# Kernel tuning notes

Measured on AMD Instinct MI355X. Metric: run time of the kernel, lower is better.

The kernel has to match this reference:

```python
import jax, jax.numpy as jnp
import numpy as np

D, NH, DH, NL, NP, NLAYERS, DFF = 256, 8, 32, 3, 4, 6, 1024
SHAPES = ((64, 64), (32, 32), (16, 16))  # (H, W) per level, strides 8/16/32 of a 512px image


def layer_norm(x, g, b):
    m = jnp.mean(x, -1, keepdims=True)
    v = jnp.mean((x - m) ** 2, -1, keepdims=True)
    return (x - m) * jax.lax.rsqrt(v + 1e-5) * g + b


def _ref_points():
    pts = []
    for (h, w) in SHAPES:
        ry = (jnp.arange(h, dtype=jnp.float32) + 0.5) / h
        rx = (jnp.arange(w, dtype=jnp.float32) + 0.5) / w
        yy, xx = jnp.meshgrid(ry, rx, indexing='ij')
        pts.append(jnp.stack([xx.reshape(-1), yy.reshape(-1)], -1))
    return jnp.concatenate(pts, 0)  # [Q, 2] (x, y) normalized; valid_ratios == 1


def _sample_level(value_l, loc, h, w):
    # value_l: [B, NH, h*w, DH]; loc: [B, Q, NH, NP, 2] normalized in [0,1]
    # grid_sample(align_corners=False, padding zeros): pixel = loc*size - 0.5
    B, Q = loc.shape[0], loc.shape[1]
    x = loc[..., 0] * w - 0.5
    y = loc[..., 1] * h - 0.5
    x0f = jnp.floor(x); y0f = jnp.floor(y)
    lx = x - x0f; ly = y - y0f
    x0 = x0f.astype(jnp.int32); y0 = y0f.astype(jnp.int32)
    out = jnp.zeros((B, NH, Q, NP, DH), value_l.dtype)
    corners = ((0, 0, (1 - lx) * (1 - ly)), (1, 0, lx * (1 - ly)),
               (0, 1, (1 - lx) * ly), (1, 1, lx * ly))
    for dx, dy, wgt in corners:
        xi = x0 + dx; yi = y0 + dy
        valid = ((xi >= 0) & (xi < w) & (yi >= 0) & (yi < h)).astype(value_l.dtype)
        idx = jnp.clip(yi, 0, h - 1) * w + jnp.clip(xi, 0, w - 1)        # [B,Q,NH,NP]
        idx_f = jnp.transpose(idx, (0, 2, 1, 3)).reshape(B, NH, Q * NP)
        v = jnp.take_along_axis(value_l, idx_f[..., None], axis=2)       # [B,NH,Q*NP,DH]
        v = v.reshape(B, NH, Q, NP, DH)
        w_f = jnp.transpose(wgt * valid, (0, 2, 1, 3))                   # [B,NH,Q,NP]
        out = out + v * w_f[..., None]
    return out


def setup_inputs():
    key = jax.random.key(0)
    ks = iter(jax.random.split(key, 64))
    d = {}
    B = 4
    for i, (h, w) in enumerate(SHAPES):
        d[f'src{i}'] = jax.random.normal(next(ks), (B, D, h, w), jnp.float32)
        d[f'pos{i}'] = jax.random.normal(next(ks), (B, D, h, w), jnp.float32) * 0.1
    s = 0.02
    p = lambda shape: jax.random.normal(next(ks), shape, jnp.float32) * s
    d['level_embed'] = p((NL, D))
    d['W_off'] = p((NLAYERS, D, NH * NL * NP * 2)); d['b_off'] = p((NLAYERS, NH * NL * NP * 2))
    d['W_attn'] = p((NLAYERS, D, NH * NL * NP));   d['b_attn'] = p((NLAYERS, NH * NL * NP))
    d['W_val'] = p((NLAYERS, D, D)); d['b_val'] = p((NLAYERS, D))
    d['W_out'] = p((NLAYERS, D, D)); d['b_out'] = p((NLAYERS, D))
    d['ln1_g'] = jnp.ones((NLAYERS, D)); d['ln1_b'] = jnp.zeros((NLAYERS, D))
    d['W_ff1'] = p((NLAYERS, D, DFF)); d['b_ff1'] = p((NLAYERS, DFF))
    d['W_ff2'] = p((NLAYERS, DFF, D)); d['b_ff2'] = p((NLAYERS, D))
    d['ln2_g'] = jnp.ones((NLAYERS, D)); d['ln2_b'] = jnp.zeros((NLAYERS, D))
    return d


def reference(src0, src1, src2, pos0, pos1, pos2, level_embed,
              W_off, b_off, W_attn, b_attn, W_val, b_val, W_out, b_out,
              ln1_g, ln1_b, W_ff1, b_ff1, W_ff2, b_ff2, ln2_g, ln2_b):
    srcs = (src0, src1, src2)
    poss = (pos0, pos1, pos2)
    B = src0.shape[0]
    # flatten levels: [B, C, H, W] -> [B, H*W, C]; add per-level embedding to pos
    src = jnp.concatenate([s.reshape(B, D, -1).transpose(0, 2, 1) for s in srcs], 1)
    pos = jnp.concatenate([poss[l].reshape(B, D, -1).transpose(0, 2, 1) + level_embed[l]
                           for l in range(NL)], 1)
    Q = src.shape[1]
    ref = _ref_points()  # [Q, 2]
    x = src
    for i in range(NLAYERS):
        q = x + pos
        off = (q @ W_off[i] + b_off[i]).reshape(B, Q, NH, NL, NP, 2)
        aw = jax.nn.softmax((q @ W_attn[i] + b_attn[i]).reshape(B, Q, NH, NL * NP), -1)
        aw = aw.reshape(B, Q, NH, NL, NP)
        val = (x @ W_val[i] + b_val[i]).reshape(B, Q, NH, DH)
        attn_out = jnp.zeros((B, Q, NH, DH), x.dtype)
        start = 0
        for l, (h, w) in enumerate(SHAPES):
            hw = h * w
            v_l = jnp.transpose(val[:, start:start + hw], (0, 2, 1, 3))  # [B,NH,hw,DH]
            wh = jnp.array([w, h], jnp.float32)
            loc = ref[None, :, None, None, :] + off[:, :, :, l] / wh     # [B,Q,NH,NP,2]
            smp = _sample_level(v_l, loc, h, w)                          # [B,NH,Q,NP,DH]
            attn_out = attn_out + jnp.einsum('bhqpd,bqhp->bqhd', smp, aw[:, :, :, l])
            start += hw
        attn_out = attn_out.reshape(B, Q, D) @ W_out[i] + b_out[i]
        x = layer_norm(x + attn_out, ln1_g[i], ln1_b[i])
        ff = jax.nn.relu(x @ W_ff1[i] + b_ff1[i]) @ W_ff2[i] + b_ff2[i]
        x = layer_norm(x + ff, ln2_g[i], ln2_b[i])
    return x  # memory: [B, Q, D]
```

## Files before the change

### kernel.cpp

```cpp
#include <hip/hip_runtime.h>


#define DMODEL 256
#define NLAYERS 6
#define BATCH 4
#define QTOT 5376
#define MROWS (BATCH * QTOT)

typedef __bf16 bf16x8 __attribute__((ext_vector_type(8)));
typedef __bf16 bf16x4 __attribute__((ext_vector_type(4)));
typedef float floatx4 __attribute__((ext_vector_type(4)));

__global__ __launch_bounds__(256) void flatten_kernel(
    const float* __restrict__ s0, const float* __restrict__ p0,
    const float* __restrict__ s1, const float* __restrict__ p1,
    const float* __restrict__ s2, const float* __restrict__ p2,
    const float* __restrict__ lvl, float* __restrict__ x,
    float* __restrict__ pos, __bf16* __restrict__ xb,
    __bf16* __restrict__ qb) {
  __shared__ float ls[32][33];
  __shared__ float lp[32][33];
  int b = blockIdx.y;
  int tile = blockIdx.x;
  const float* sp; const float* pp; int l, hw, tp, td, qbase;
  if (tile < 1024)      { l = 0; hw = 4096; int t = tile;        td = t & 7; tp = t >> 3; qbase = 0; sp = s0; pp = p0; }
  else if (tile < 1280) { l = 1; hw = 1024; int t = tile - 1024; td = t & 7; tp = t >> 3; qbase = 4096; sp = s1; pp = p1; }
  else                  { l = 2; hw = 256;  int t = tile - 1280; td = t & 7; tp = t >> 3; qbase = 5120; sp = s2; pp = p2; }
  int tx = threadIdx.x & 31, ty = threadIdx.x >> 5;
  int d0 = td * 32, pbase = tp * 32;
#pragma unroll
  for (int r = 0; r < 4; ++r) {
    int dl = r * 8 + ty;
    size_t gi = ((size_t)(b * DMODEL + d0 + dl)) * hw + pbase + tx;
    ls[dl][tx] = sp[gi];
    lp[dl][tx] = pp[gi];
  }
  __syncthreads();
  int d = d0 + tx;
  float lv = lvl[l * DMODEL + d];
#pragma unroll
  for (int r = 0; r < 4; ++r) {
    int pl = r * 8 + ty;
    size_t bq = (size_t)b * QTOT + qbase + pbase + pl;
    float xv = ls[tx][pl];
    float pv = lp[tx][pl] + lv;
    x[bq * DMODEL + d] = xv;
    xb[bq * DMODEL + d] = (__bf16)xv;
    pos[bq * DMODEL + d] = pv;
    qb[bq * DMODEL + d] = (__bf16)(xv + pv);
  }
}

__global__ __launch_bounds__(256) void pack_wt_kernel(
    const float* __restrict__ W, __bf16* __restrict__ Wt, int K, int N) {
  int l = blockIdx.y;
  int idx = blockIdx.x * 256 + threadIdx.x;
  int n = idx / K, k = idx - n * K;
  Wt[(size_t)l * N * K + idx] = (__bf16)W[(size_t)l * K * N + (size_t)k * N + n];
}

__global__ __launch_bounds__(256) void pack_qv_kernel(
    const float* __restrict__ Woff, const float* __restrict__ Wattn,
    const float* __restrict__ Wval,
    const float* __restrict__ boff, const float* __restrict__ battn,
    const float* __restrict__ bval,
    __bf16* __restrict__ Wt, float* __restrict__ bc) {
  int l = blockIdx.y;
  int n = blockIdx.x;
  int k = threadIdx.x;
  float v = 0.f;
  if (n < 192)      v = Woff[((size_t)l * 256 + k) * 192 + n];
  else if (n < 288) v = Wattn[((size_t)l * 256 + k) * 96 + (n - 192)];
  else if (n >= 384) v = Wval[((size_t)l * 256 + k) * 256 + (n - 384)];
  Wt[((size_t)l * 640 + n) * 256 + k] = (__bf16)v;
  if (k == 0) {
    float b = 0.f;
    if (n < 192)      b = boff[l * 192 + n];
    else if (n < 288) b = battn[l * 96 + (n - 192)];
    else if (n >= 384) b = bval[l * 256 + (n - 384)];
    bc[l * 640 + n] = b;
  }
}

#define GEMM_CORE(A_, B_, K_)                                                  \
  for (int k0 = 0; k0 < (K_); k0 += 32) {                                      \
    __syncthreads();                                                           \
    _Pragma("unroll")                                                          \
    for (int cc = 0; cc < 2; ++cc) {                                           \
      int c = wid * 2 + cc;                                                    \
      __builtin_amdgcn_global_load_lds(                                        \
          (__attribute__((address_space(1))) void*)((A_) + (size_t)c * 16 * (K_) + k0), \
          (__attribute__((address_space(3))) void*)(As + c * 512), 16, 0, 0);  \
      __builtin_amdgcn_global_load_lds(                                        \
          (__attribute__((address_space(1))) void*)((B_) + (size_t)c * 16 * (K_) + k0), \
          (__attribute__((address_space(3))) void*)(Bs + c * 512), 16, 0, 0);  \
    }                                                                          \
    __syncthreads();                                                           \
    bf16x8 af[4], bfr[4];                                                      \
    _Pragma("unroll")                                                          \
    for (int i = 0; i < 4; ++i)                                                \
      af[i] = *(const bf16x8*)&As[(wr * 64 + i * 16 + (lane & 15)) * 32 + (lane >> 4) * 8]; \
    _Pragma("unroll")                                                          \
    for (int j = 0; j < 4; ++j)                                                \
      bfr[j] = *(const bf16x8*)&Bs[(wc * 64 + j * 16 + (lane & 15)) * 32 + (lane >> 4) * 8]; \
    _Pragma("unroll")                                                          \
    for (int i = 0; i < 4; ++i)                                                \
      _Pragma("unroll")                                                        \
      for (int j = 0; j < 4; ++j)                                              \
        acc[i][j] = __builtin_amdgcn_mfma_f32_16x16x32_bf16(af[i], bfr[j], acc[i][j], 0, 0, 0); \
  }

template<int RELU, int BF16OUT>
__global__ __launch_bounds__(256) void gemm_bf16_kernel(
    const __bf16* __restrict__ A, const __bf16* __restrict__ Wt,
    const float* __restrict__ bias, float* __restrict__ C,
    __bf16* __restrict__ Cb, int N, int K) {
  __shared__ __bf16 As[128 * 32];
  __shared__ __bf16 Bs[128 * 32];
  int t = threadIdx.x;
  int lane = t & 63, wid = t >> 6;
  int wr = wid >> 1, wc = wid & 1;
  int row0 = blockIdx.y * 128;
  int n0 = blockIdx.x * 128;
  floatx4 acc[4][4] = {};
  int srow = lane >> 2;
  int skoff = (lane & 3) * 8;
  const __bf16* Abase = A + (size_t)(row0 + srow) * K + skoff;
  const __bf16* Bbase = Wt + (size_t)(n0 + srow) * K + skoff;
  GEMM_CORE(Abase, Bbase, K)
  int orow = row0 + wr * 64 + (lane >> 4) * 4;
  int ocol = n0 + wc * 64 + (lane & 15);
#pragma unroll
  for (int i = 0; i < 4; ++i)
#pragma unroll
    for (int j = 0; j < 4; ++j) {
      int col = ocol + j * 16;
      float bv = bias[col];
#pragma unroll
      for (int r = 0; r < 4; ++r) {
        int row = orow + i * 16 + r;
        float v = acc[i][j][r] + bv;
        if (RELU) v = fmaxf(v, 0.f);
        if (BF16OUT) Cb[(size_t)row * N + col] = (__bf16)v;
        else         C[(size_t)row * N + col] = v;
      }
    }
}

__global__ __launch_bounds__(256) void gemm_qv_kernel(
    const __bf16* __restrict__ qb, const __bf16* __restrict__ xb,
    const __bf16* __restrict__ Wt, const float* __restrict__ bias,
    float* __restrict__ qproj, __bf16* __restrict__ valb) {
  __shared__ __bf16 As[128 * 32];
  __shared__ __bf16 Bs[128 * 32];
  int t = threadIdx.x;
  int lane = t & 63, wid = t >> 6;
  int wr = wid >> 1, wc = wid & 1;
  int bn = blockIdx.x;
  int row0 = blockIdx.y * 128;
  int n0 = bn * 128;
  const __bf16* A = (bn < 3) ? qb : xb;
  floatx4 acc[4][4] = {};
  int srow = lane >> 2;
  int skoff = (lane & 3) * 8;
  const __bf16* Abase = A + (size_t)(row0 + srow) * 256 + skoff;
  const __bf16* Bbase = Wt + (size_t)(n0 + srow) * 256 + skoff;
  GEMM_CORE(Abase, Bbase, 256)
  int orow = row0 + wr * 64 + (lane >> 4) * 4;
  int ocol = wc * 64 + (lane & 15);
#pragma unroll
  for (int i = 0; i < 4; ++i)
#pragma unroll
    for (int j = 0; j < 4; ++j) {
      int col = ocol + j * 16;
      float bv = bias[n0 + col];
#pragma unroll
      for (int r = 0; r < 4; ++r) {
        int row = orow + i * 16 + r;
        float v = acc[i][j][r] + bv;
        if (bn < 3) qproj[(size_t)row * 384 + n0 + col] = v;
        else        valb[(size_t)row * 256 + (n0 - 384) + col] = (__bf16)v;
      }
    }
}

__global__ __launch_bounds__(256) void deform_kernel(
    const __bf16* __restrict__ val, const float* __restrict__ qproj,
    __bf16* __restrict__ out) {
  int bq = blockIdx.x * 8 + (threadIdx.x >> 5);
  int b = bq / QTOT, q = bq % QTOT;
  int tq = threadIdx.x & 31;
  int hid = tq >> 2, dq = (tq & 3) * 8;

  int p, wsrc;
  if (q < 4096)      { p = q;        wsrc = 64; }
  else if (q < 5120) { p = q - 4096; wsrc = 32; }
  else               { p = q - 5120; wsrc = 16; }
  float inv = 1.0f / (float)wsrc;
  float refx = ((float)(p % wsrc) + 0.5f) * inv;
  float refy = ((float)(p / wsrc) + 0.5f) * inv;

  const float* base = qproj + (size_t)bq * 384;
  float aw[12], ob[24];
  *(float4*)&aw[0] = *(const float4*)(base + 192 + hid * 12);
  *(float4*)&aw[4] = *(const float4*)(base + 192 + hid * 12 + 4);
  *(float4*)&aw[8] = *(const float4*)(base + 192 + hid * 12 + 8);
#pragma unroll
  for (int i = 0; i < 6; ++i)
    *(float4*)&ob[i * 4] = *(const float4*)(base + hid * 24 + i * 4);

  float mx = -1e30f;
#pragma unroll
  for (int k = 0; k < 12; ++k) mx = fmaxf(mx, aw[k]);
  float s = 0.f;
#pragma unroll
  for (int k = 0; k < 12; ++k) { aw[k] = __expf(aw[k] - mx); s += aw[k]; }
  float invs = 1.0f / s;
#pragma unroll
  for (int k = 0; k < 12; ++k) aw[k] *= invs;

  const __bf16* vb = val + ((size_t)b * QTOT) * DMODEL + hid * 32 + dq;

  const int starts[3] = {0, 4096, 5120};
  const int wls[3] = {64, 32, 16};
  float acc[8] = {};
#pragma unroll
  for (int l = 0; l < 3; ++l) {
    int wl = wls[l], start = starts[l];
    float fwl = (float)wl;
#pragma unroll
    for (int pp = 0; pp < 4; ++pp) {
      float wcomb = aw[l * 4 + pp];
      float fx = refx * fwl + ob[(l * 4 + pp) * 2 + 0] - 0.5f;
      float fy = refy * fwl + ob[(l * 4 + pp) * 2 + 1] - 0.5f;
      float x0f = floorf(fx), y0f = floorf(fy);
      float lx = fx - x0f, ly = fy - y0f;
      int x0 = (int)x0f, y0 = (int)y0f;
#pragma unroll
      for (int c = 0; c < 4; ++c) {
        int dx = c & 1, dy = c >> 1;
        int xi = x0 + dx, yi = y0 + dy;
        if (xi >= 0 && xi < wl && yi >= 0 && yi < wl) {
          float wgt = (dx ? lx : 1.f - lx) * (dy ? ly : 1.f - ly) * wcomb;
          bf16x8 v = *(const bf16x8*)(vb + (size_t)(start + yi * wl + xi) * DMODEL);
#pragma unroll
          for (int e = 0; e < 8; ++e)
            acc[e] = fmaf(wgt, (float)v[e], acc[e]);
        }
      }
    }
  }
  bf16x8 o;
#pragma unroll
  for (int e = 0; e < 8; ++e) o[e] = (__bf16)acc[e];
  *(bf16x8*)(out + (size_t)bq * DMODEL + hid * 32 + dq) = o;
}

__global__ __launch_bounds__(256) void add_ln_kernel(
    const float* __restrict__ x, const float* __restrict__ res,
    const float* __restrict__ g, const float* __restrict__ bta,
    float* __restrict__ xout, __bf16* __restrict__ xb,
    const float* __restrict__ pos, __bf16* __restrict__ qb) {
  int row = blockIdx.x * 4 + (threadIdx.x >> 6);
  int lane = threadIdx.x & 63;
  float4 xv = ((const float4*)(x + (size_t)row * DMODEL))[lane];
  float4 rv = ((const float4*)(res + (size_t)row * DMODEL))[lane];
  xv.x += rv.x; xv.y += rv.y; xv.z += rv.z; xv.w += rv.w;
  float s = xv.x + xv.y + xv.z + xv.w;
  float sq = xv.x * xv.x + xv.y * xv.y + xv.z * xv.z + xv.w * xv.w;
#pragma unroll
  for (int o = 32; o >= 1; o >>= 1) {
    s += __shfl_xor(s, o);
    sq += __shfl_xor(sq, o);
  }
  float mean = s * (1.f / 256.f);
  float var = sq * (1.f / 256.f) - mean * mean;
  float rstd = rsqrtf(var + 1e-5f);
  int c = lane * 4;
  float4 gv = *(const float4*)(g + c);
  float4 bv = *(const float4*)(bta + c);
  float4 o4;
  o4.x = (xv.x - mean) * rstd * gv.x + bv.x;
  o4.y = (xv.y - mean) * rstd * gv.y + bv.y;
  o4.z = (xv.z - mean) * rstd * gv.z + bv.z;
  o4.w = (xv.w - mean) * rstd * gv.w + bv.w;
  ((float4*)(xout + (size_t)row * DMODEL))[lane] = o4;
  bf16x4 ob;
  ob[0] = (__bf16)o4.x; ob[1] = (__bf16)o4.y;
  ob[2] = (__bf16)o4.z; ob[3] = (__bf16)o4.w;
  *(bf16x4*)&xb[(size_t)row * DMODEL + c] = ob;
  if (pos) {
    float4 pv = ((const float4*)(pos + (size_t)row * DMODEL))[lane];
    bf16x4 qv;
    qv[0] = (__bf16)(o4.x + pv.x); qv[1] = (__bf16)(o4.y + pv.y);
    qv[2] = (__bf16)(o4.z + pv.z); qv[3] = (__bf16)(o4.w + pv.w);
    *(bf16x4*)&qb[(size_t)row * DMODEL + c] = qv;
  }
}

extern "C" void kernel_launch(void* const* d_in, const int* in_sizes, int n_in,
                              void* d_out, int out_size, void* d_ws, size_t ws_size,
                              hipStream_t stream) {
  const float* src0 = (const float*)d_in[0];
  const float* pos0 = (const float*)d_in[1];
  const float* src1 = (const float*)d_in[2];
  const float* pos1 = (const float*)d_in[3];
  const float* src2 = (const float*)d_in[4];
  const float* pos2 = (const float*)d_in[5];
  const float* lvl  = (const float*)d_in[6];
  const float* W_off  = (const float*)d_in[7];
  const float* b_off  = (const float*)d_in[8];
  const float* W_attn = (const float*)d_in[9];
  const float* b_attn = (const float*)d_in[10];
  const float* W_val  = (const float*)d_in[11];
  const float* b_val  = (const float*)d_in[12];
  const float* W_out  = (const float*)d_in[13];
  const float* b_out  = (const float*)d_in[14];
  const float* ln1g = (const float*)d_in[15];
  const float* ln1b = (const float*)d_in[16];
  const float* W_ff1 = (const float*)d_in[17];
  const float* b_ff1 = (const float*)d_in[18];
  const float* W_ff2 = (const float*)d_in[19];
  const float* b_ff2 = (const float*)d_in[20];
  const float* ln2g = (const float*)d_in[21];
  const float* ln2b = (const float*)d_in[22];

  const size_t M = (size_t)MROWS;
  char* w = (char*)d_ws;
  float*  x     = (float*)w;                 w += M * 256 * 4;
  float*  pos   = (float*)w;                 w += M * 256 * 4;
  __bf16* xb    = (__bf16*)w;                w += M * 256 * 2;
  __bf16* qb    = (__bf16*)w;                w += M * 256 * 2;
  float*  qproj = (float*)w;                 w += M * 384 * 4;
  __bf16* valb  = (__bf16*)w;                w += M * 256 * 2;
  __bf16* ffh   = (__bf16*)w;                w += M * 1024 * 2;
  __bf16* wqv_t = (__bf16*)w;                w += (size_t)NLAYERS * 640 * 256 * 2;
  __bf16* wout_t= (__bf16*)w;                w += (size_t)NLAYERS * 256 * 256 * 2;
  __bf16* wff1_t= (__bf16*)w;                w += (size_t)NLAYERS * 1024 * 256 * 2;
  __bf16* wff2_t= (__bf16*)w;                w += (size_t)NLAYERS * 256 * 1024 * 2;
  float*  bqv   = (float*)w;                 w += (size_t)NLAYERS * 640 * 4;
  __bf16* attn_bf = qb;
  float*  proj  = (float*)ffh;
  float*  ffres = qproj;

  pack_qv_kernel<<<dim3(640, NLAYERS), 256, 0, stream>>>(
      W_off, W_attn, W_val, b_off, b_attn, b_val, wqv_t, bqv);
  pack_wt_kernel<<<dim3(256, NLAYERS), 256, 0, stream>>>(W_out, wout_t, 256, 256);
  pack_wt_kernel<<<dim3(1024, NLAYERS), 256, 0, stream>>>(W_ff1, wff1_t, 256, 1024);
  pack_wt_kernel<<<dim3(1024, NLAYERS), 256, 0, stream>>>(W_ff2, wff2_t, 1024, 256);

  flatten_kernel<<<dim3(1344, BATCH), 256, 0, stream>>>(
      src0, pos0, src1, pos1, src2, pos2, lvl, x, pos, xb, qb);

  const int MT = MROWS / 128;
  for (int i = 0; i < NLAYERS; ++i) {
    gemm_qv_kernel<<<dim3(5, MT), 256, 0, stream>>>(
        qb, xb, wqv_t + (size_t)i * 640 * 256, bqv + i * 640, qproj, valb);
    deform_kernel<<<MROWS / 8, 256, 0, stream>>>(valb, qproj, attn_bf);
    gemm_bf16_kernel<0, 0><<<dim3(2, MT), 256, 0, stream>>>(
        attn_bf, wout_t + (size_t)i * 256 * 256, b_out + i * 256, proj, nullptr, 256, 256);
    add_ln_kernel<<<MROWS / 4, 256, 0, stream>>>(
        x, proj, ln1g + i * 256, ln1b + i * 256, x, xb, nullptr, nullptr);
    gemm_bf16_kernel<1, 1><<<dim3(8, MT), 256, 0, stream>>>(
        xb, wff1_t + (size_t)i * 1024 * 256, b_ff1 + i * 1024, nullptr, ffh, 1024, 256);
    gemm_bf16_kernel<0, 0><<<dim3(2, MT), 256, 0, stream>>>(
        ffh, wff2_t + (size_t)i * 256 * 1024, b_ff2 + i * 256, ffres, nullptr, 256, 1024);
    float* xdst = (i == NLAYERS - 1) ? (float*)d_out : x;
    add_ln_kernel<<<MROWS / 4, 256, 0, stream>>>(
        x, ffres, ln2g + i * 256, ln2b + i * 256, xdst, xb, pos, qb);
  }
}
```

Measured before the change: 1.017 ms.

## Fuse residual add and LayerNorm into full-row output GEMM epilogues

Replaces the out-projection and FF2 GEMMs plus their separate add+LayerNorm kernels with one kernel whose 64x256 tile covers a whole row. It adds bias and residual, reduces the row statistics across waves through LDS, and writes the fp32, bf16 and query outputs directly. This removes the fp32 intermediate round-trips and two launches per layer. The weight packing kernels are also rewritten as LDS-tiled transposes for coalesced access. The 64-row tiles give the output GEMMs a different occupancy and reuse balance, and xout may alias xin.

Measured after the change: 1.088 ms. 6.9% more time.

```diff
diff --git a/kernel.cpp b/kernel.cpp
--- a/kernel.cpp
+++ b/kernel.cpp
@@ -10,6 +10,11 @@
 typedef __bf16 bf16x8 __attribute__((ext_vector_type(8)));
 typedef __bf16 bf16x4 __attribute__((ext_vector_type(4)));
 typedef float floatx4 __attribute__((ext_vector_type(4)));
+
+#define GLOAD(gp, lp)                                                          \
+  __builtin_amdgcn_global_load_lds(                                            \
+      (__attribute__((address_space(1))) void*)(gp),                           \
+      (__attribute__((address_space(3))) void*)(lp), 16, 0, 0)
 
 __global__ __launch_bounds__(256) void flatten_kernel(
     const float* __restrict__ s0, const float* __restrict__ p0,
@@ -51,35 +56,54 @@
   }
 }
 
-__global__ __launch_bounds__(256) void pack_wt_kernel(
+__global__ __launch_bounds__(256) void pack_t_kernel(
     const float* __restrict__ W, __bf16* __restrict__ Wt, int K, int N) {
-  int l = blockIdx.y;
-  int idx = blockIdx.x * 256 + threadIdx.x;
-  int n = idx / K, k = idx - n * K;
-  Wt[(size_t)l * N * K + idx] = (__bf16)W[(size_t)l * K * N + (size_t)k * N + n];
-}
-
-__global__ __launch_bounds__(256) void pack_qv_kernel(
+  __shared__ float ls[32][33];
+  int l = blockIdx.z;
+  int n0 = blockIdx.x * 32, k0 = blockIdx.y * 32;
+  int tx = threadIdx.x & 31, ty = threadIdx.x >> 5;
+  const float* src = W + (size_t)l * K * N;
+#pragma unroll
+  for (int r = 0; r < 4; ++r)
+    ls[ty + r * 8][tx] = src[(size_t)(k0 + ty + r * 8) * N + n0 + tx];
+  __syncthreads();
+  __bf16* dst = Wt + (size_t)l * N * K;
+#pragma unroll
+  for (int r = 0; r < 4; ++r)
+    dst[(size_t)(n0 + ty + r * 8) * K + k0 + tx] = (__bf16)ls[tx][ty + r * 8];
+}
+
+__global__ __launch_bounds__(256) void pack_qv_t_kernel(
     const float* __restrict__ Woff, const float* __restrict__ Wattn,
-    const float* __restrict__ Wval,
+    const float* __restrict__ Wval, __bf16* __restrict__ Wt) {
+  __shared__ float ls[32][33];
+  int l = blockIdx.z;
+  int tc = blockIdx.x, k0 = blockIdx.y * 32;
+  int tx = threadIdx.x & 31, ty = threadIdx.x >> 5;
+  const float* src; int n0, sn;
+  if (tc < 6)       { src = Woff  + (size_t)l * 256 * 192; n0 = tc * 32;        sn = 192; }
+  else if (tc < 9)  { src = Wattn + (size_t)l * 256 * 96;  n0 = (tc - 6) * 32;  sn = 96;  }
+  else if (tc < 12) { src = nullptr; n0 = 0; sn = 0; }
+  else              { src = Wval  + (size_t)l * 256 * 256; n0 = (tc - 12) * 32; sn = 256; }
+#pragma unroll
+  for (int r = 0; r < 4; ++r)
+    ls[ty + r * 8][tx] = src ? src[(size_t)(k0 + ty + r * 8) * sn + n0 + tx] : 0.f;
+  __syncthreads();
+  __bf16* dst = Wt + (size_t)l * 640 * 256 + (size_t)tc * 32 * 256;
+#pragma unroll
+  for (int r = 0; r < 4; ++r)
+    dst[(size_t)(ty + r * 8) * 256 + k0 + tx] = (__bf16)ls[tx][ty + r * 8];
+}
+
+__global__ __launch_bounds__(640) void pack_bias_kernel(
     const float* __restrict__ boff, const float* __restrict__ battn,
-    const float* __restrict__ bval,
-    __bf16* __restrict__ Wt, float* __restrict__ bc) {
-  int l = blockIdx.y;
-  int n = blockIdx.x;
-  int k = threadIdx.x;
-  float v = 0.f;
-  if (n < 192)      v = Woff[((size_t)l * 256 + k) * 192 + n];
-  else if (n < 288) v = Wattn[((size_t)l * 256 + k) * 96 + (n - 192)];
-  else if (n >= 384) v = Wval[((size_t)l * 256 + k) * 256 + (n - 384)];
-  Wt[((size_t)l * 640 + n) * 256 + k] = (__bf16)v;
-  if (k == 0) {
-    float b = 0.f;
-    if (n < 192)      b = boff[l * 192 + n];
-    else if (n < 288) b = battn[l * 96 + (n - 192)];
-    else if (n >= 384) b = bval[l * 256 + (n - 384)];
-    bc[l * 640 + n] = b;
-  }
+    const float* __restrict__ bval, float* __restrict__ bc) {
+  int l = blockIdx.x, n = threadIdx.x;
+  float b = 0.f;
+  if (n < 192)       b = boff[l * 192 + n];
+  else if (n < 288)  b = battn[l * 96 + (n - 192)];
+  else if (n >= 384) b = bval[l * 256 + (n - 384)];
+  bc[l * 640 + n] = b;
 }
 
 #define GEMM_CORE(A_, B_, K_)                                                  \
@@ -88,12 +112,8 @@
     _Pragma("unroll")                                                          \
     for (int cc = 0; cc < 2; ++cc) {                                           \
       int c = wid * 2 + cc;                                                    \
-      __builtin_amdgcn_global_load_lds(                                        \
-          (__attribute__((address_space(1))) void*)((A_) + (size_t)c * 16 * (K_) + k0), \
-          (__attribute__((address_space(3))) void*)(As + c * 512), 16, 0, 0);  \
-      __builtin_amdgcn_global_load_lds(                                        \
-          (__attribute__((address_space(1))) void*)((B_) + (size_t)c * 16 * (K_) + k0), \
-          (__attribute__((address_space(3))) void*)(Bs + c * 512), 16, 0, 0);  \
+      GLOAD((A_) + (size_t)c * 16 * (K_) + k0, As + c * 512);                  \
+      GLOAD((B_) + (size_t)c * 16 * (K_) + k0, Bs + c * 512);                  \
     }                                                                          \
     __syncthreads();                                                           \
     bf16x8 af[4], bfr[4];                                                      \
@@ -184,6 +204,111 @@
     }
 }
 
+template<int QB, int KK>
+__global__ __launch_bounds__(256) void gemm_ln_kernel(
+    const __bf16* __restrict__ A, const __bf16* __restrict__ Wt,
+    const float* __restrict__ bias, const float* __restrict__ xin,
+    const float* __restrict__ g, const float* __restrict__ bta,
+    float* __restrict__ xout, __bf16* __restrict__ xb,
+    const float* __restrict__ pos, __bf16* __restrict__ qb) {
+  __shared__ __bf16 As[64 * 32];
+  __shared__ __bf16 Bs[256 * 32];
+  __shared__ float stats[64][2];
+  int t = threadIdx.x, lane = t & 63, wid = t >> 6;
+  int row0 = blockIdx.x * 64;
+  floatx4 acc[4][4] = {};
+  int srow = lane >> 2, skoff = (lane & 3) * 8;
+  const __bf16* Abase = A + (size_t)(row0 + srow) * KK + skoff;
+  const __bf16* Bbase = Wt + (size_t)srow * KK + skoff;
+
+  for (int k0 = 0; k0 < KK; k0 += 32) {
+    __syncthreads();
+#pragma unroll
+    for (int cc = 0; cc < 5; ++cc) {
+      int c = wid * 5 + cc;
+      if (c < 4) GLOAD(Abase + (size_t)c * 16 * KK + k0, As + c * 512);
+      else       GLOAD(Bbase + (size_t)(c - 4) * 16 * KK + k0, Bs + (c - 4) * 512);
+    }
+    __syncthreads();
+    bf16x8 af[4], bfr[4];
+#pragma unroll
+    for (int i = 0; i < 4; ++i)
+      af[i] = *(const bf16x8*)&As[(i * 16 + (lane & 15)) * 32 + (lane >> 4) * 8];
+#pragma unroll
+    for (int j = 0; j < 4; ++j)
+      bfr[j] = *(const bf16x8*)&Bs[(wid * 64 + j * 16 + (lane & 15)) * 32 + (lane >> 4) * 8];
+#pragma unroll
+    for (int i = 0; i < 4; ++i)
+#pragma unroll
+      for (int j = 0; j < 4; ++j)
+        acc[i][j] = __builtin_amdgcn_mfma_f32_16x16x32_bf16(af[i], bfr[j], acc[i][j], 0, 0, 0);
+  }
+
+  __syncthreads();
+  float* part = (float*)As;
+
+  int lr0 = (lane >> 4) * 4;
+  int colbase = wid * 64 + (lane & 15);
+  float psum[4][4] = {}, psq[4][4] = {};
+#pragma unroll
+  for (int i = 0; i < 4; ++i)
+#pragma unroll
+    for (int j = 0; j < 4; ++j) {
+      int col = colbase + j * 16;
+      float bv = bias[col];
+#pragma unroll
+      for (int r = 0; r < 4; ++r) {
+        int lr = lr0 + i * 16 + r;
+        float v = acc[i][j][r] + bv + xin[(size_t)(row0 + lr) * DMODEL + col];
+        acc[i][j][r] = v;
+        psum[i][r] += v;
+        psq[i][r] += v * v;
+      }
+    }
+#pragma unroll
+  for (int o = 1; o < 16; o <<= 1)
+#pragma unroll
+    for (int i = 0; i < 4; ++i)
+#pragma unroll
+      for (int r = 0; r < 4; ++r) {
+        psum[i][r] += __shfl_xor(psum[i][r], o);
+        psq[i][r]  += __shfl_xor(psq[i][r], o);
+      }
+  {
+    int m = lane & 15, i = m >> 2, r = m & 3;
+    int lr = lr0 + i * 16 + r;
+    part[lr * 8 + wid]     = psum[i][r];
+    part[lr * 8 + 4 + wid] = psq[i][r];
+  }
+  __syncthreads();
+  if (t < 64) {
+    float s = part[t * 8 + 0] + part[t * 8 + 1] + part[t * 8 + 2] + part[t * 8 + 3];
+    float q = part[t * 8 + 4] + part[t * 8 + 5] + part[t * 8 + 6] + part[t * 8 + 7];
+    float mean = s * (1.f / 256.f);
+    float var = q * (1.f / 256.f) - mean * mean;
+    stats[t][0] = mean;
+    stats[t][1] = rsqrtf(var + 1e-5f);
+  }
+  __syncthreads();
+#pragma unroll
+  for (int i = 0; i < 4; ++i)
+#pragma unroll
+    for (int j = 0; j < 4; ++j) {
+      int col = colbase + j * 16;
+      float gv = g[col], bv = bta[col];
+#pragma unroll
+      for (int r = 0; r < 4; ++r) {
+        int lr = lr0 + i * 16 + r;
+        float mean = stats[lr][0], rstd = stats[lr][1];
+        float o = (acc[i][j][r] - mean) * rstd * gv + bv;
+        size_t idx = (size_t)(row0 + lr) * DMODEL + col;
+        xout[idx] = o;
+        xb[idx] = (__bf16)o;
+        if (QB) qb[idx] = (__bf16)(o + pos[idx]);
+      }
+    }
+}
+
 __global__ __launch_bounds__(256) void deform_kernel(
     const __bf16* __restrict__ val, const float* __restrict__ qproj,
     __bf16* __restrict__ out) {
@@ -254,48 +379,6 @@
 #pragma unroll
   for (int e = 0; e < 8; ++e) o[e] = (__bf16)acc[e];
   *(bf16x8*)(out + (size_t)bq * DMODEL + hid * 32 + dq) = o;
-}
-
-__global__ __launch_bounds__(256) void add_ln_kernel(
-    const float* __restrict__ x, const float* __restrict__ res,
-    const float* __restrict__ g, const float* __restrict__ bta,
-    float* __restrict__ xout, __bf16* __restrict__ xb,
-    const float* __restrict__ pos, __bf16* __restrict__ qb) {
-  int row = blockIdx.x * 4 + (threadIdx.x >> 6);
-  int lane = threadIdx.x & 63;
-  float4 xv = ((const float4*)(x + (size_t)row * DMODEL))[lane];
-  float4 rv = ((const float4*)(res + (size_t)row * DMODEL))[lane];
-  xv.x += rv.x; xv.y += rv.y; xv.z += rv.z; xv.w += rv.w;
-  float s = xv.x + xv.y + xv.z + xv.w;
-  float sq = xv.x * xv.x + xv.y * xv.y + xv.z * xv.z + xv.w * xv.w;
-#pragma unroll
-  for (int o = 32; o >= 1; o >>= 1) {
-    s += __shfl_xor(s, o);
-    sq += __shfl_xor(sq, o);
-  }
-  float mean = s * (1.f / 256.f);
-  float var = sq * (1.f / 256.f) - mean * mean;
-  float rstd = rsqrtf(var + 1e-5f);
-  int c = lane * 4;
-  float4 gv = *(const float4*)(g + c);
-  float4 bv = *(const float4*)(bta + c);
-  float4 o4;
-  o4.x = (xv.x - mean) * rstd * gv.x + bv.x;
-  o4.y = (xv.y - mean) * rstd * gv.y + bv.y;
-  o4.z = (xv.z - mean) * rstd * gv.z + bv.z;
-  o4.w = (xv.w - mean) * rstd * gv.w + bv.w;
-  ((float4*)(xout + (size_t)row * DMODEL))[lane] = o4;
-  bf16x4 ob;
-  ob[0] = (__bf16)o4.x; ob[1] = (__bf16)o4.y;
-  ob[2] = (__bf16)o4.z; ob[3] = (__bf16)o4.w;
-  *(bf16x4*)&xb[(size_t)row * DMODEL + c] = ob;
-  if (pos) {
-    float4 pv = ((const float4*)(pos + (size_t)row * DMODEL))[lane];
-    bf16x4 qv;
-    qv[0] = (__bf16)(o4.x + pv.x); qv[1] = (__bf16)(o4.y + pv.y);
-    qv[2] = (__bf16)(o4.z + pv.z); qv[3] = (__bf16)(o4.w + pv.w);
-    *(bf16x4*)&qb[(size_t)row * DMODEL + c] = qv;
-  }
 }
 
 extern "C" void kernel_launch(void* const* d_in, const int* in_sizes, int n_in,
@@ -340,33 +423,30 @@
   __bf16* wff2_t= (__bf16*)w;                w += (size_t)NLAYERS * 256 * 1024 * 2;
   float*  bqv   = (float*)w;                 w += (size_t)NLAYERS * 640 * 4;
   __bf16* attn_bf = qb;
-  float*  proj  = (float*)ffh;
-  float*  ffres = qproj;
-
-  pack_qv_kernel<<<dim3(640, NLAYERS), 256, 0, stream>>>(
-      W_off, W_attn, W_val, b_off, b_attn, b_val, wqv_t, bqv);
-  pack_wt_kernel<<<dim3(256, NLAYERS), 256, 0, stream>>>(W_out, wout_t, 256, 256);
-  pack_wt_kernel<<<dim3(1024, NLAYERS), 256, 0, stream>>>(W_ff1, wff1_t, 256, 1024);
-  pack_wt_kernel<<<dim3(1024, NLAYERS), 256, 0, stream>>>(W_ff2, wff2_t, 1024, 256);
+
+  pack_qv_t_kernel<<<dim3(20, 8, NLAYERS), 256, 0, stream>>>(W_off, W_attn, W_val, wqv_t);
+  pack_bias_kernel<<<NLAYERS, 640, 0, stream>>>(b_off, b_attn, b_val, bqv);
+  pack_t_kernel<<<dim3(8, 8, NLAYERS), 256, 0, stream>>>(W_out, wout_t, 256, 256);
+  pack_t_kernel<<<dim3(32, 8, NLAYERS), 256, 0, stream>>>(W_ff1, wff1_t, 256, 1024);
+  pack_t_kernel<<<dim3(8, 32, NLAYERS), 256, 0, stream>>>(W_ff2, wff2_t, 1024, 256);
 
   flatten_kernel<<<dim3(1344, BATCH), 256, 0, stream>>>(
       src0, pos0, src1, pos1, src2, pos2, lvl, x, pos, xb, qb);
 
   const int MT = MROWS / 128;
+  const int LT = MROWS / 64;
   for (int i = 0; i < NLAYERS; ++i) {
     gemm_qv_kernel<<<dim3(5, MT), 256, 0, stream>>>(
         qb, xb, wqv_t + (size_t)i * 640 * 256, bqv + i * 640, qproj, valb);
     deform_kernel<<<MROWS / 8, 256, 0, stream>>>(valb, qproj, attn_bf);
-    gemm_bf16_kernel<0, 0><<<dim3(2, MT), 256, 0, stream>>>(
-        attn_bf, wout_t + (size_t)i * 256 * 256, b_out + i * 256, proj, nullptr, 256, 256);
-    add_ln_kernel<<<MROWS / 4, 256, 0, stream>>>(
-        x, proj, ln1g + i * 256, ln1b + i * 256, x, xb, nullptr, nullptr);
+    gemm_ln_kernel<0, 256><<<LT, 256, 0, stream>>>(
+        attn_bf, wout_t + (size_t)i * 256 * 256, b_out + i * 256,
+        x, ln1g + i * 256, ln1b + i * 256, x, xb, nullptr, nullptr);
     gemm_bf16_kernel<1, 1><<<dim3(8, MT), 256, 0, stream>>>(
         xb, wff1_t + (size_t)i * 1024 * 256, b_ff1 + i * 1024, nullptr, ffh, 1024, 256);
-    gemm_bf16_kernel<0, 0><<<dim3(2, MT), 256, 0, stream>>>(
-        ffh, wff2_t + (size_t)i * 256 * 1024, b_ff2 + i * 256, ffres, nullptr, 256, 1024);
     float* xdst = (i == NLAYERS - 1) ? (float*)d_out : x;
-    add_ln_kernel<<<MROWS / 4, 256, 0, stream>>>(
-        x, ffres, ln2g + i * 256, ln2b + i * 256, xdst, xb, pos, qb);
-  }
-}
+    gemm_ln_kernel<1, 1024><<<LT, 256, 0, stream>>>(
+        ffh, wff2_t + (size_t)i * 256 * 1024, b_ff2 + i * 256,
+        x, ln2g + i * 256, ln2b + i * 256, xdst, xb, pos, qb);
+  }
+}
```
